# Kernel tuning notes

Hardware: AMD Instinct MI355X
Metric: run time of the kernel (lower is better)

## Reference

```python
import jax, jax.numpy as jnp
import numpy as np

B, S, D, H = 4, 2048, 1024, 16  # batch, seq, d_hidden, n_heads


def setup_inputs() -> dict:
    key = jax.random.key(0)
    ks = jax.random.split(key, 7)
    scale = 1.0 / np.sqrt(D)
    return {
        "x": jax.random.normal(ks[0], (B, S, D), dtype=jnp.float32),
        "Wq": jax.random.normal(ks[1], (D, D), dtype=jnp.float32) * scale,
        "bq": jax.random.normal(ks[2], (D,), dtype=jnp.float32) * 0.02,
        "Wk": jax.random.normal(ks[3], (D, D), dtype=jnp.float32) * scale,
        "bk": jax.random.normal(ks[4], (D,), dtype=jnp.float32) * 0.02,
        "Wv": jax.random.normal(ks[5], (D, D), dtype=jnp.float32) * scale,
        "bv": jax.random.normal(ks[6], (D,), dtype=jnp.float32) * 0.02,
    }


def reference(x, Wq, bq, Wk, bk, Wv, bv):
    n_heads = H
    head_dim = D // n_heads

    def proj(inp, W, b):
        # torch nn.Linear: y = x @ W^T + b
        y = jnp.einsum("bsd,ed->bse", inp, W) + b
        # split last dim into (H, Wd) then transpose to (B, H, S, Wd)
        return y.reshape(inp.shape[0], inp.shape[1], n_heads, head_dim).transpose(0, 2, 1, 3)

    q = proj(x, Wq, bq)
    k = proj(x, Wk, bk)
    v = proj(x, Wv, bv)

    # scores: (B, H, S, S)
    scores = jnp.einsum("bhqd,bhkd->bhqk", q, k) / jnp.sqrt(jnp.asarray(head_dim, q.dtype))
    attn = jax.nn.softmax(scores, axis=-1)
    h = jnp.einsum("bhqk,bhkd->bhqd", attn, v)  # (B, H, S, Wd)
    h = h.transpose(0, 2, 1, 3).reshape(x.shape[0], x.shape[1], D)  # merge heads
    return h
```

## Files before the change

kernel.cpp:

```cpp
#include <hip/hip_runtime.h>
#include <hip/hip_bf16.h>

#define B_ 4
#define S_ 2048
#define D_ 1024
#define H_ 16
#define HD 64

typedef __bf16 bf16;
typedef __bf16 bf16x4 __attribute__((ext_vector_type(4)));
typedef __bf16 bf16x8 __attribute__((ext_vector_type(8)));
typedef float f32x4 __attribute__((ext_vector_type(4)));
typedef float f32x16 __attribute__((ext_vector_type(16)));

#define LOG2E 1.4426950408889634f

__device__ inline void gload_lds16(const bf16* g, bf16* l) {
    __builtin_amdgcn_global_load_lds(
        (const __attribute__((address_space(1))) void*)g,
        (__attribute__((address_space(3))) void*)l, 16, 0, 0);
}

__device__ inline int swz(int row, int colb) {
    return row * 64 + ((colb ^ ((row & 7) << 4)) >> 1);
}

__device__ inline unsigned cvt_pk_bf16(float lo, float hi) {
    unsigned r;
    asm("v_cvt_pk_bf16_f32 %0, %1, %2" : "=v"(r) : "v"(lo), "v"(hi));
    return r;
}

__global__ void cast_pack_kernel(const float* __restrict__ x,
                                 const float* __restrict__ Wq,
                                 const float* __restrict__ Wk,
                                 const float* __restrict__ Wv,
                                 bf16* __restrict__ Xb, bf16* __restrict__ Wb) {
    const long XN = (long)B_ * S_ * D_;
    const long WN = (long)D_ * D_;
    long i4 = ((long)blockIdx.x * blockDim.x + threadIdx.x) * 4;
    if (i4 < XN) {
        float4 v = *(const float4*)(x + i4);
        bf16* o = Xb + i4;
        o[0] = (bf16)v.x; o[1] = (bf16)v.y; o[2] = (bf16)v.z; o[3] = (bf16)v.w;
    } else {
        long j = i4 - XN;
        if (j < 3 * WN) {
            int which = (int)(j / WN);
            long jj = j - (long)which * WN;
            const float* src = which == 0 ? Wq : which == 1 ? Wk : Wv;
            float4 v = *(const float4*)(src + jj);
            bf16* o = Wb + j;
            o[0] = (bf16)v.x; o[1] = (bf16)v.y; o[2] = (bf16)v.z; o[3] = (bf16)v.w;
        }
    }
}

#define TM 128
#define TN 256
#define TK 64

__global__ __launch_bounds__(512, 2) void gemm_qkv_kernel(
    const bf16* __restrict__ Xb, const bf16* __restrict__ Wb,
    const float* __restrict__ bq, const float* __restrict__ bk,
    const float* __restrict__ bv,
    bf16* __restrict__ Qg, bf16* __restrict__ Kg, bf16* __restrict__ Vt) {
    __shared__ bf16 SMEM[49152];
    bf16* As = SMEM;
    bf16* Bs = SMEM + 16384;
    const int tid = threadIdx.x;
    const int lane = tid & 63;
    const int wid = tid >> 6;
    const int col = lane & 15, grp = lane >> 4;
    const int wr = wid >> 2, wc = wid & 3;

    const int id = blockIdx.x;
    const int id2 = (id & 7) * 96 + (id >> 3);
    const int m0 = (id2 / 12) * TM;
    const int n0 = (id2 % 12) * TN;

    const int r8 = tid >> 3;
    const int cbs = ((tid & 7) * 16) ^ ((r8 & 7) << 4);
    const bf16* asrc = Xb + (size_t)(m0 + r8) * D_ + (cbs >> 1);
    const bf16* bsrc = Wb + (size_t)(n0 + r8) * D_ + (cbs >> 1);

#define STAGE_A(c, kt, j) \
    gload_lds16(asrc + (size_t)(j) * 64 * D_ + (kt) * TK, As + (c) * 8192 + (j) * 4096 + wid * 512)
#define STAGE_B(c, kt, j) \
    gload_lds16(bsrc + (size_t)(j) * 64 * D_ + (kt) * TK, Bs + (c) * 16384 + (j) * 4096 + wid * 512)

    const f32x4 zf = {0.f, 0.f, 0.f, 0.f};
    f32x4 acc[4][4];
#pragma unroll
    for (int m = 0; m < 4; m++)
#pragma unroll
        for (int n = 0; n < 4; n++) acc[m][n] = zf;

    STAGE_A(0, 0, 0); STAGE_A(0, 0, 1);
    STAGE_B(0, 0, 0); STAGE_B(0, 0, 1); STAGE_B(0, 0, 2); STAGE_B(0, 0, 3);
    asm volatile("s_waitcnt vmcnt(0)");
    __builtin_amdgcn_s_barrier();

    int c = 0;
#pragma unroll 1
    for (int kt = 0; kt < D_ / TK; ++kt) {
        const bf16* Ac = As + c * 8192;
        const bf16* Bc = Bs + c * 16384;
        {
            bf16x8 a[4], b[4];
#pragma unroll
            for (int m = 0; m < 4; m++)
                a[m] = *(const bf16x8*)(Ac + swz(wr * 64 + m * 16 + col, grp * 16));
#pragma unroll
            for (int n = 0; n < 4; n++)
                b[n] = *(const bf16x8*)(Bc + swz(wc * 64 + n * 16 + col, grp * 16));
            if (kt < D_ / TK - 1) {
                STAGE_A(c ^ 1, kt + 1, 0); STAGE_A(c ^ 1, kt + 1, 1);
                STAGE_B(c ^ 1, kt + 1, 0);
            }
            __builtin_amdgcn_s_barrier();
            asm volatile("s_waitcnt lgkmcnt(0)");
            __builtin_amdgcn_sched_barrier(0);
            __builtin_amdgcn_s_setprio(1);
#pragma unroll
            for (int m = 0; m < 4; m++)
#pragma unroll
                for (int n = 0; n < 4; n++)
                    acc[m][n] = __builtin_amdgcn_mfma_f32_16x16x32_bf16(a[m], b[n], acc[m][n], 0, 0, 0);
            __builtin_amdgcn_s_setprio(0);
            __builtin_amdgcn_s_barrier();
        }
        {
            bf16x8 a[4], b[4];
#pragma unroll
            for (int m = 0; m < 4; m++)
                a[m] = *(const bf16x8*)(Ac + swz(wr * 64 + m * 16 + col, 64 + grp * 16));
#pragma unroll
            for (int n = 0; n < 4; n++)
                b[n] = *(const bf16x8*)(Bc + swz(wc * 64 + n * 16 + col, 64 + grp * 16));
            if (kt < D_ / TK - 1) {
                STAGE_B(c ^ 1, kt + 1, 1); STAGE_B(c ^ 1, kt + 1, 2); STAGE_B(c ^ 1, kt + 1, 3);
            }
            __builtin_amdgcn_s_barrier();
            asm volatile("s_waitcnt lgkmcnt(0)");
            __builtin_amdgcn_sched_barrier(0);
            __builtin_amdgcn_s_setprio(1);
#pragma unroll
            for (int m = 0; m < 4; m++)
#pragma unroll
                for (int n = 0; n < 4; n++)
                    acc[m][n] = __builtin_amdgcn_mfma_f32_16x16x32_bf16(a[m], b[n], acc[m][n], 0, 0, 0);
            __builtin_amdgcn_s_setprio(0);
            asm volatile("s_waitcnt vmcnt(0)");
            __builtin_amdgcn_s_barrier();
        }
        c ^= 1;
    }
#undef STAGE_A
#undef STAGE_B

    const int which = n0 >> 10;
    if (which == 2) {
        __syncthreads();
        bf16* Vl = SMEM;
#pragma unroll
        for (int n = 0; n < 4; n++) {
            int dl = wc * 64 + n * 16 + col;
            float bias = bv[(n0 - 2048) + dl];
#pragma unroll
            for (int m = 0; m < 4; m++) {
                bf16x4 pv;
#pragma unroll
                for (int i = 0; i < 4; i++) pv[i] = (bf16)(acc[m][n][i] + bias);
                int sl = wr * 64 + m * 16 + grp * 4;
                *(bf16x4*)(&Vl[dl * 128 + (sl ^ ((dl & 7) << 3))]) = pv;
            }
        }
        __syncthreads();
#pragma unroll
        for (int c0 = 0; c0 < 8; c0++) {
            int cc = c0 * 512 + tid;
            int dl = cc >> 4, s8 = (cc & 15) * 8;
            bf16x8 val = *(const bf16x8*)(&Vl[dl * 128 + (s8 ^ ((dl & 7) << 3))]);
            int s = m0 + s8;
            int b = s >> 11, sl = s & 2047;
            int dglob = (n0 - 2048) + dl;
            int h = dglob >> 6, dd = dglob & 63;
            *(bf16x8*)(&Vt[((size_t)(b * H_ + h) * HD + dd) * S_ + sl]) = val;
        }
    } else {
        const float* bp = which == 0 ? bq : bk;
        bf16* dst = which == 0 ? Qg : Kg;
        const float qsc = which == 0 ? (0.125f * LOG2E) : 1.0f;
#pragma unroll
        for (int n = 0; n < 4; n++) {
            int e = n0 + wc * 64 + n * 16 + col;
            int ee = e & 1023;
            float bias = bp[ee];
            int h = ee >> 6, d = ee & 63;
#pragma unroll
            for (int m = 0; m < 4; m++) {
#pragma unroll
                for (int i = 0; i < 4; i++) {
                    int s = m0 + wr * 64 + m * 16 + grp * 4 + i;
                    int b = s >> 11, sl = s & 2047;
                    dst[((size_t)(b * H_ + h) * S_ + sl) * HD + d] =
                        (bf16)((acc[m][n][i] + bias) * qsc);
                }
            }
        }
    }
}

#define KB 64

__global__ __launch_bounds__(512, 4) void attn_kernel(
    const bf16* __restrict__ Qg, const bf16* __restrict__ Kg,
    const bf16* __restrict__ Vt, float* __restrict__ out) {
    __shared__ bf16 Ks[2][64 * 64];
    __shared__ bf16 Vs[2][64 * 64];
    const int tid = threadIdx.x, lane = tid & 63, wid = tid >> 6;
    const int l31 = lane & 31, hi = lane >> 5;

    const int id = blockIdx.x;
    const int swzid = (id & 7) * 64 + (id >> 3);
    const int bh = swzid >> 3;
    const int q0 = (swzid & 7) * 256 + wid * 32;

    const bf16* Kbase = Kg + (size_t)bh * S_ * HD;
    const bf16* Vbase = Vt + (size_t)bh * HD * S_;

    const int r0 = tid >> 3;
    const int cb = ((tid & 7) * 16) ^ ((r0 & 7) << 4);
    const bf16* ksrc = Kbase + (size_t)r0 * HD + (cb >> 1);
    const bf16* vsrc = Vbase + (size_t)r0 * S_ + (cb >> 1);

#define STAGE(bsel, kv0)                                            \
    do {                                                            \
        gload_lds16(ksrc + (size_t)(kv0)*HD, &Ks[bsel][wid * 512]); \
        gload_lds16(vsrc + (kv0), &Vs[bsel][wid * 512]);            \
    } while (0)

    bf16x8 qa[4];
#pragma unroll
    for (int ks = 0; ks < 4; ks++)
        qa[ks] = *(const bf16x8*)(Qg + ((size_t)bh * S_ + q0 + l31) * HD + ks * 16 + hi * 8);

    const f32x16 z16 = {0.f, 0.f, 0.f, 0.f, 0.f, 0.f, 0.f, 0.f,
                        0.f, 0.f, 0.f, 0.f, 0.f, 0.f, 0.f, 0.f};
    f32x16 o[2];
    o[0] = z16; o[1] = z16;
    f32x4 ls = {0.f, 0.f, 0.f, 0.f};

    int cur = 0;
    STAGE(0, 0);
    __syncthreads();

    for (int t = 0; t < S_ / KB; ++t) {
        if (t < S_ / KB - 1) STAGE(cur ^ 1, (t + 1) * KB);

        f32x16 sc[2];
        __builtin_amdgcn_s_setprio(1);
#pragma unroll
        for (int kvt = 0; kvt < 2; kvt++) {
            {
                bf16x8 kb = *(const bf16x8*)(&Ks[cur][swz(kvt * 32 + l31, hi * 16)]);
                sc[kvt] = __builtin_amdgcn_mfma_f32_32x32x16_bf16(kb, qa[0], z16, 0, 0, 0);
            }
#pragma unroll
            for (int ks = 1; ks < 4; ks++) {
                bf16x8 kb = *(const bf16x8*)(&Ks[cur][swz(kvt * 32 + l31, ks * 32 + hi * 16)]);
                sc[kvt] = __builtin_amdgcn_mfma_f32_32x32x16_bf16(kb, qa[ks], sc[kvt], 0, 0, 0);
            }
        }
        __builtin_amdgcn_s_setprio(0);

        bf16x8 pa[4];
#pragma unroll
        for (int kvt = 0; kvt < 2; kvt++) {
            float p[16];
#pragma unroll
            for (int r = 0; r < 16; r++) p[r] = __builtin_amdgcn_exp2f(sc[kvt][r]);
            f32x4 s0 = {p[0], p[1], p[2], p[3]};
            f32x4 s1 = {p[4], p[5], p[6], p[7]};
            f32x4 s2 = {p[8], p[9], p[10], p[11]};
            f32x4 s3 = {p[12], p[13], p[14], p[15]};
            ls += (s0 + s1) + (s2 + s3);
#pragma unroll
            for (int b = 0; b < 2; b++) {
                unsigned A  = cvt_pk_bf16(p[8 * b + 0], p[8 * b + 1]);
                unsigned Bw = cvt_pk_bf16(p[8 * b + 4], p[8 * b + 5]);
                unsigned C  = cvt_pk_bf16(p[8 * b + 2], p[8 * b + 3]);
                unsigned Dw = cvt_pk_bf16(p[8 * b + 6], p[8 * b + 7]);
                asm("v_permlane32_swap_b32 %0, %1" : "+v"(A), "+v"(Bw));
                asm("v_permlane32_swap_b32 %0, %1" : "+v"(C), "+v"(Dw));
                union { unsigned u[4]; bf16x8 v; } pk;
                pk.u[0] = A; pk.u[1] = C; pk.u[2] = Bw; pk.u[3] = Dw;
                pa[kvt * 2 + b] = pk.v;
            }
        }

        __builtin_amdgcn_s_setprio(1);
#pragma unroll
        for (int ks2 = 0; ks2 < 4; ks2++) {
#pragma unroll
            for (int dt = 0; dt < 2; dt++) {
                bf16x8 vb = *(const bf16x8*)(&Vs[cur][swz(dt * 32 + l31, ks2 * 32 + hi * 16)]);
                o[dt] = __builtin_amdgcn_mfma_f32_32x32x16_bf16(vb, pa[ks2], o[dt], 0, 0, 0);
            }
        }
        __builtin_amdgcn_s_setprio(0);

        __syncthreads();
        cur ^= 1;
    }

    float denom = ls[0] + ls[1] + ls[2] + ls[3];
    denom += __shfl_xor(denom, 32);
    float inv = 1.f / denom;

    int b = bh >> 4, h = bh & 15;
    int q = q0 + l31;
    float* obase = out + ((size_t)(b * S_ + q)) * D_ + h * HD;
#pragma unroll
    for (int dt = 0; dt < 2; dt++)
#pragma unroll
        for (int g = 0; g < 4; g++) {
            f32x4 r = {o[dt][4 * g + 0] * inv, o[dt][4 * g + 1] * inv,
                       o[dt][4 * g + 2] * inv, o[dt][4 * g + 3] * inv};
            *(f32x4*)(obase + dt * 32 + 8 * g + 4 * hi) = r;
        }
#undef STAGE
}

extern "C" void kernel_launch(void* const* d_in, const int* in_sizes, int n_in,
                              void* d_out, int out_size, void* d_ws, size_t ws_size,
                              hipStream_t stream) {
    const float* x  = (const float*)d_in[0];
    const float* Wq = (const float*)d_in[1];
    const float* bq = (const float*)d_in[2];
    const float* Wk = (const float*)d_in[3];
    const float* bk = (const float*)d_in[4];
    const float* Wv = (const float*)d_in[5];
    const float* bv = (const float*)d_in[6];
    float* out = (float*)d_out;

    bf16* ws = (bf16*)d_ws;
    bf16* Xb = ws;
    bf16* Wb = Xb + (size_t)B_ * S_ * D_;
    bf16* Qg = Wb + (size_t)3 * D_ * D_;
    bf16* Kg = Qg + (size_t)B_ * S_ * D_;
    bf16* Vt = Kg + (size_t)B_ * S_ * D_;

    hipLaunchKernelGGL(cast_pack_kernel,
                       dim3((B_ * S_ * D_ + 3 * D_ * D_) / (4 * 256)), dim3(256), 0, stream,
                       x, Wq, Wk, Wv, Xb, Wb);
    hipLaunchKernelGGL(gemm_qkv_kernel, dim3(64 * 12), dim3(512), 0, stream,
                       Xb, Wb, bq, bk, bv, Qg, Kg, Vt);
    hipLaunchKernelGGL(attn_kernel, dim3(512), dim3(512), 0, stream,
                       Qg, Kg, Vt, out);
}
```

Baseline: 159.4 us.

## Give each attention wave two 32-row query tiles with 256-thread blocks

New measurement: 158.7 us (median of 2 runs). About the same (-0.4%).

```diff
diff --git a/kernel.cpp b/kernel.cpp
--- a/kernel.cpp
+++ b/kernel.cpp
@@ -214,7 +214,7 @@
 
 #define KB 64
 
-__global__ __launch_bounds__(512, 4) void attn_kernel(
+__global__ __launch_bounds__(256, 2) void attn_kernel(
     const bf16* __restrict__ Qg, const bf16* __restrict__ Kg,
     const bf16* __restrict__ Vt, float* __restrict__ out) {
     __shared__ bf16 Ks[2][64 * 64];
@@ -225,7 +225,7 @@
     const int id = blockIdx.x;
     const int swzid = (id & 7) * 64 + (id >> 3);
     const int bh = swzid >> 3;
-    const int q0 = (swzid & 7) * 256 + wid * 32;
+    const int q0w = (swzid & 7) * 256 + wid * 64;
 
     const bf16* Kbase = Kg + (size_t)bh * S_ * HD;
     const bf16* Vbase = Vt + (size_t)bh * HD * S_;
@@ -235,22 +235,26 @@
     const bf16* ksrc = Kbase + (size_t)r0 * HD + (cb >> 1);
     const bf16* vsrc = Vbase + (size_t)r0 * S_ + (cb >> 1);
 
-#define STAGE(bsel, kv0)                                            \
-    do {                                                            \
-        gload_lds16(ksrc + (size_t)(kv0)*HD, &Ks[bsel][wid * 512]); \
-        gload_lds16(vsrc + (kv0), &Vs[bsel][wid * 512]);            \
+#define STAGE(bsel, kv0)                                                       \
+    do {                                                                       \
+        gload_lds16(ksrc + (size_t)(kv0)*HD,        &Ks[bsel][wid * 512]);     \
+        gload_lds16(ksrc + (size_t)((kv0) + 32)*HD, &Ks[bsel][2048 + wid * 512]); \
+        gload_lds16(vsrc + (kv0),                   &Vs[bsel][wid * 512]);     \
+        gload_lds16(vsrc + 32 * S_ + (kv0),         &Vs[bsel][2048 + wid * 512]); \
     } while (0)
 
-    bf16x8 qa[4];
-#pragma unroll
-    for (int ks = 0; ks < 4; ks++)
-        qa[ks] = *(const bf16x8*)(Qg + ((size_t)bh * S_ + q0 + l31) * HD + ks * 16 + hi * 8);
+    bf16x8 qa[2][4];
+#pragma unroll
+    for (int qs = 0; qs < 2; qs++)
+#pragma unroll
+        for (int ks = 0; ks < 4; ks++)
+            qa[qs][ks] = *(const bf16x8*)(Qg + ((size_t)bh * S_ + q0w + qs * 32 + l31) * HD + ks * 16 + hi * 8);
 
     const f32x16 z16 = {0.f, 0.f, 0.f, 0.f, 0.f, 0.f, 0.f, 0.f,
                         0.f, 0.f, 0.f, 0.f, 0.f, 0.f, 0.f, 0.f};
-    f32x16 o[2];
-    o[0] = z16; o[1] = z16;
-    f32x4 ls = {0.f, 0.f, 0.f, 0.f};
+    f32x16 o[2][2];
+    o[0][0] = z16; o[0][1] = z16; o[1][0] = z16; o[1][1] = z16;
+    f32x4 ls[2] = {{0.f, 0.f, 0.f, 0.f}, {0.f, 0.f, 0.f, 0.f}};
 
     int cur = 0;
     STAGE(0, 0);
@@ -259,77 +263,89 @@
     for (int t = 0; t < S_ / KB; ++t) {
         if (t < S_ / KB - 1) STAGE(cur ^ 1, (t + 1) * KB);
 
-        f32x16 sc[2];
+        f32x16 sc[2][2];
         __builtin_amdgcn_s_setprio(1);
 #pragma unroll
         for (int kvt = 0; kvt < 2; kvt++) {
-            {
-                bf16x8 kb = *(const bf16x8*)(&Ks[cur][swz(kvt * 32 + l31, hi * 16)]);
-                sc[kvt] = __builtin_amdgcn_mfma_f32_32x32x16_bf16(kb, qa[0], z16, 0, 0, 0);
-            }
-#pragma unroll
-            for (int ks = 1; ks < 4; ks++) {
+#pragma unroll
+            for (int ks = 0; ks < 4; ks++) {
                 bf16x8 kb = *(const bf16x8*)(&Ks[cur][swz(kvt * 32 + l31, ks * 32 + hi * 16)]);
-                sc[kvt] = __builtin_amdgcn_mfma_f32_32x32x16_bf16(kb, qa[ks], sc[kvt], 0, 0, 0);
+                if (ks == 0) {
+                    sc[0][kvt] = __builtin_amdgcn_mfma_f32_32x32x16_bf16(kb, qa[0][0], z16, 0, 0, 0);
+                    sc[1][kvt] = __builtin_amdgcn_mfma_f32_32x32x16_bf16(kb, qa[1][0], z16, 0, 0, 0);
+                } else {
+                    sc[0][kvt] = __builtin_amdgcn_mfma_f32_32x32x16_bf16(kb, qa[0][ks], sc[0][kvt], 0, 0, 0);
+                    sc[1][kvt] = __builtin_amdgcn_mfma_f32_32x32x16_bf16(kb, qa[1][ks], sc[1][kvt], 0, 0, 0);
+                }
             }
         }
         __builtin_amdgcn_s_setprio(0);
 
-        bf16x8 pa[4];
-#pragma unroll
-        for (int kvt = 0; kvt < 2; kvt++) {
-            float p[16];
-#pragma unroll
-            for (int r = 0; r < 16; r++) p[r] = __builtin_amdgcn_exp2f(sc[kvt][r]);
-            f32x4 s0 = {p[0], p[1], p[2], p[3]};
-            f32x4 s1 = {p[4], p[5], p[6], p[7]};
-            f32x4 s2 = {p[8], p[9], p[10], p[11]};
-            f32x4 s3 = {p[12], p[13], p[14], p[15]};
-            ls += (s0 + s1) + (s2 + s3);
-#pragma unroll
-            for (int b = 0; b < 2; b++) {
-                unsigned A  = cvt_pk_bf16(p[8 * b + 0], p[8 * b + 1]);
-                unsigned Bw = cvt_pk_bf16(p[8 * b + 4], p[8 * b + 5]);
-                unsigned C  = cvt_pk_bf16(p[8 * b + 2], p[8 * b + 3]);
-                unsigned Dw = cvt_pk_bf16(p[8 * b + 6], p[8 * b + 7]);
-                asm("v_permlane32_swap_b32 %0, %1" : "+v"(A), "+v"(Bw));
-                asm("v_permlane32_swap_b32 %0, %1" : "+v"(C), "+v"(Dw));
-                union { unsigned u[4]; bf16x8 v; } pk;
-                pk.u[0] = A; pk.u[1] = C; pk.u[2] = Bw; pk.u[3] = Dw;
-                pa[kvt * 2 + b] = pk.v;
-            }
-        }
-
-        __builtin_amdgcn_s_setprio(1);
-#pragma unroll
-        for (int ks2 = 0; ks2 < 4; ks2++) {
-#pragma unroll
-            for (int dt = 0; dt < 2; dt++) {
-                bf16x8 vb = *(const bf16x8*)(&Vs[cur][swz(dt * 32 + l31, ks2 * 32 + hi * 16)]);
-                o[dt] = __builtin_amdgcn_mfma_f32_32x32x16_bf16(vb, pa[ks2], o[dt], 0, 0, 0);
-            }
-        }
-        __builtin_amdgcn_s_setprio(0);
+        bf16x8 vb[2][4];
+#pragma unroll
+        for (int kk = 0; kk < 4; kk++)
+#pragma unroll
+            for (int dt = 0; dt < 2; dt++)
+                vb[dt][kk] = *(const bf16x8*)(&Vs[cur][swz(dt * 32 + l31, kk * 32 + hi * 16)]);
+
+#pragma unroll
+        for (int qs = 0; qs < 2; qs++) {
+            bf16x8 pa[4];
+#pragma unroll
+            for (int kvt = 0; kvt < 2; kvt++) {
+                float p[16];
+#pragma unroll
+                for (int r = 0; r < 16; r++) p[r] = __builtin_amdgcn_exp2f(sc[qs][kvt][r]);
+                f32x4 s0 = {p[0], p[1], p[2], p[3]};
+                f32x4 s1 = {p[4], p[5], p[6], p[7]};
+                f32x4 s2 = {p[8], p[9], p[10], p[11]};
+                f32x4 s3 = {p[12], p[13], p[14], p[15]};
+                ls[qs] += (s0 + s1) + (s2 + s3);
+#pragma unroll
+                for (int b = 0; b < 2; b++) {
+                    unsigned A  = cvt_pk_bf16(p[8 * b + 0], p[8 * b + 1]);
+                    unsigned Bw = cvt_pk_bf16(p[8 * b + 4], p[8 * b + 5]);
+                    unsigned C  = cvt_pk_bf16(p[8 * b + 2], p[8 * b + 3]);
+                    unsigned Dw = cvt_pk_bf16(p[8 * b + 6], p[8 * b + 7]);
+                    asm("v_permlane32_swap_b32 %0, %1" : "+v"(A), "+v"(Bw));
+                    asm("v_permlane32_swap_b32 %0, %1" : "+v"(C), "+v"(Dw));
+                    union { unsigned u[4]; bf16x8 v; } pk;
+                    pk.u[0] = A; pk.u[1] = C; pk.u[2] = Bw; pk.u[3] = Dw;
+                    pa[kvt * 2 + b] = pk.v;
+                }
+            }
+
+            __builtin_amdgcn_s_setprio(1);
+#pragma unroll
+            for (int kk = 0; kk < 4; kk++) {
+#pragma unroll
+                for (int dt = 0; dt < 2; dt++)
+                    o[qs][dt] = __builtin_amdgcn_mfma_f32_32x32x16_bf16(vb[dt][kk], pa[kk], o[qs][dt], 0, 0, 0);
+            }
+            __builtin_amdgcn_s_setprio(0);
+        }
 
         __syncthreads();
         cur ^= 1;
     }
 
-    float denom = ls[0] + ls[1] + ls[2] + ls[3];
-    denom += __shfl_xor(denom, 32);
-    float inv = 1.f / denom;
-
     int b = bh >> 4, h = bh & 15;
-    int q = q0 + l31;
-    float* obase = out + ((size_t)(b * S_ + q)) * D_ + h * HD;
-#pragma unroll
-    for (int dt = 0; dt < 2; dt++)
-#pragma unroll
-        for (int g = 0; g < 4; g++) {
-            f32x4 r = {o[dt][4 * g + 0] * inv, o[dt][4 * g + 1] * inv,
-                       o[dt][4 * g + 2] * inv, o[dt][4 * g + 3] * inv};
-            *(f32x4*)(obase + dt * 32 + 8 * g + 4 * hi) = r;
-        }
+#pragma unroll
+    for (int qs = 0; qs < 2; qs++) {
+        float denom = ls[qs][0] + ls[qs][1] + ls[qs][2] + ls[qs][3];
+        denom += __shfl_xor(denom, 32);
+        float inv = 1.f / denom;
+        int q = q0w + qs * 32 + l31;
+        float* obase = out + ((size_t)(b * S_ + q)) * D_ + h * HD;
+#pragma unroll
+        for (int dt = 0; dt < 2; dt++)
+#pragma unroll
+            for (int g = 0; g < 4; g++) {
+                f32x4 r = {o[qs][dt][4 * g + 0] * inv, o[qs][dt][4 * g + 1] * inv,
+                           o[qs][dt][4 * g + 2] * inv, o[qs][dt][4 * g + 3] * inv};
+                *(f32x4*)(obase + dt * 32 + 8 * g + 4 * hi) = r;
+            }
+    }
 #undef STAGE
 }
 
@@ -357,6 +373,6 @@
                        x, Wq, Wk, Wv, Xb, Wb);
     hipLaunchKernelGGL(gemm_qkv_kernel, dim3(64 * 12), dim3(512), 0, stream,
                        Xb, Wb, bq, bk, bv, Qg, Kg, Vt);
-    hipLaunchKernelGGL(attn_kernel, dim3(512), dim3(512), 0, stream,
+    hipLaunchKernelGGL(attn_kernel, dim3(512), dim3(256), 0, stream,
                        Qg, Kg, Vt, out);
 }
```
